# Optimization experiments

Hardware: AMD Instinct MI355X
Metric: run time of the kernel (lower is better)

The kernel has to match this reference:

```python
import jax, jax.numpy as jnp
import numpy as np

KERNEL_SIZE = 5
SIGMA_INTENSITY = 0.1
SIGMA_SPATIAL = 1.0
EPS = 1e-8


def make_spatial_kernel():
    coords = jnp.arange(KERNEL_SIZE, dtype=jnp.float32) - KERNEL_SIZE // 2
    x, y = jnp.meshgrid(coords, coords, indexing='ij')
    return jnp.exp(-(x ** 2 + y ** 2) / (2.0 * SIGMA_SPATIAL ** 2))


def setup_inputs() -> dict:
    key = jax.random.key(0)
    images = jax.random.uniform(key, (16, 3, 512, 512), dtype=jnp.float32)
    spatial_kernel = make_spatial_kernel()
    return {"images": images, "spatial_kernel": spatial_kernel}


def reference(images, spatial_kernel):
    B, C, H, W = images.shape
    K = KERNEL_SIZE
    p = K // 2
    # reflect pad (torch 'reflect' == jnp 'reflect', edge not repeated)
    padded = jnp.pad(images, ((0, 0), (0, 0), (p, p), (p, p)), mode='reflect')
    # extract K*K shifted views -> (B, C, K*K, H, W); fixed small loop over offsets
    patches = jnp.stack(
        [padded[:, :, i:i + H, j:j + W] for i in range(K) for j in range(K)],
        axis=2,
    )
    center_idx = K * K // 2
    center = patches[:, :, center_idx:center_idx + 1, :, :]
    diff = patches - center
    intensity_w = jnp.exp(-(diff ** 2) / (2.0 * SIGMA_INTENSITY ** 2))
    spatial_flat = spatial_kernel.reshape(1, 1, K * K, 1, 1)
    w = spatial_flat * intensity_w
    w = w / (jnp.sum(w, axis=2, keepdims=True) + EPS)
    filtered = jnp.sum(patches * w, axis=2)  # (B, C, H, W)
    return filtered
```

## Files before the change

kernel.cpp:

```cpp
#include <hip/hip_runtime.h>

#define TILE_W 64
#define TILE_H 4
#define HALO   2
#define LW     (TILE_W + 2*HALO)
#define LH     (TILE_H + 2*HALO)
#define IMG    512

__device__ __forceinline__ int reflect_idx(int g) {
    int a = abs(g);
    return min(a, 2 * IMG - 2 - a);
}

#define KS      8.4932184f
#define INV_KS  0.11774083f
#define L2E_HLF 0.72134752f

__global__ __launch_bounds__(256) void bilateral_kernel(
    const float* __restrict__ img, float* __restrict__ out, int planes)
{
    __shared__ float q[LH][LW];

    const int plane = blockIdx.z;
    const int x0 = blockIdx.x * TILE_W;
    const int y0 = blockIdx.y * TILE_H;
    const float* __restrict__ src = img + (size_t)plane * (IMG * IMG);

    const int tid = threadIdx.x + threadIdx.y * TILE_W;

    #pragma unroll
    for (int i = 0; i < 3; ++i) {
        int idx = tid + i * 256;
        if (idx < LH * LW) {
            int r = idx / LW;
            int c = idx - r * LW;
            int gr = reflect_idx(y0 - HALO + r);
            int gc = reflect_idx(x0 - HALO + c);
            q[r][c] = src[gr * IMG + gc] * KS;
        }
    }
    __syncthreads();

    const int tx = threadIdx.x, ty = threadIdx.y;
    const float qc = q[ty + HALO][tx + HALO];

    float wsum = 0.0f, acc = 0.0f;
    #pragma unroll
    for (int dy = 0; dy < 5; ++dy) {
        #pragma unroll
        for (int dx = 0; dx < 5; ++dx) {
            const float ctap = -(float)((dx - 2) * (dx - 2) + (dy - 2) * (dy - 2)) * L2E_HLF;
            float qt  = q[ty + dy][tx + dx];
            float d   = qt - qc;
            float arg = __builtin_fmaf(-d, d, ctap);
            float e   = __builtin_amdgcn_exp2f(arg);
            wsum += e;
            acc = __builtin_fmaf(e, qt, acc);
        }
    }

    float inv = __builtin_amdgcn_rcpf(wsum + 1e-8f);
    out[(size_t)plane * (IMG * IMG) + (size_t)(y0 + ty) * IMG + (x0 + tx)] =
        acc * inv * INV_KS;
}

extern "C" void kernel_launch(void* const* d_in, const int* in_sizes, int n_in,
                              void* d_out, int out_size, void* d_ws, size_t ws_size,
                              hipStream_t stream) {
    const float* img = (const float*)d_in[0];
    float* out = (float*)d_out;
    int planes = in_sizes[0] / (IMG * IMG);
    dim3 grid(IMG / TILE_W, IMG / TILE_H, planes);
    dim3 block(TILE_W, TILE_H, 1);
    bilateral_kernel<<<grid, block, 0, stream>>>(img, out, planes);
}
```

Measured before the change: 150.3 us.

## Compute four rows per thread with register window and packed float2 math

Each thread now produces four vertically adjacent outputs, using a taller tile (16 rows) that loads more halo once per block. Each thread loads an 8x5 window from shared memory into registers and reuses it across its rows. The arithmetic is done on float2 vectors so the compiler can emit packed FP32 ops, and the centre tap is skipped because its weight is known to be 1. The aim is to cut LDS traffic, halo overhead and ALU instructions, at the cost of more registers per thread and fewer blocks.

```diff
diff --git a/kernel.cpp b/kernel.cpp
--- a/kernel.cpp
+++ b/kernel.cpp
@@ -1,11 +1,14 @@
 #include <hip/hip_runtime.h>
 
-#define TILE_W 64
-#define TILE_H 4
-#define HALO   2
-#define LW     (TILE_W + 2*HALO)
-#define LH     (TILE_H + 2*HALO)
-#define IMG    512
+#define IMG  512
+#define TW   64
+#define TH   16
+#define RPT  4
+#define HALO 2
+#define LW   (TW + 2*HALO)
+#define LH   (TH + 2*HALO)
+
+typedef float v2f __attribute__((ext_vector_type(2)));
 
 __device__ __forceinline__ int reflect_idx(int g) {
     int a = abs(g);
@@ -17,51 +20,75 @@
 #define L2E_HLF 0.72134752f
 
 __global__ __launch_bounds__(256) void bilateral_kernel(
-    const float* __restrict__ img, float* __restrict__ out, int planes)
+    const float* __restrict__ img, float* __restrict__ out)
 {
     __shared__ float q[LH][LW];
 
     const int plane = blockIdx.z;
-    const int x0 = blockIdx.x * TILE_W;
-    const int y0 = blockIdx.y * TILE_H;
+    const int x0 = blockIdx.x * TW;
+    const int y0 = blockIdx.y * TH;
     const float* __restrict__ src = img + (size_t)plane * (IMG * IMG);
 
-    const int tid = threadIdx.x + threadIdx.y * TILE_W;
+    const int tid = threadIdx.x + threadIdx.y * 64;
 
     #pragma unroll
-    for (int i = 0; i < 3; ++i) {
+    for (int i = 0; i < 6; ++i) {
         int idx = tid + i * 256;
         if (idx < LH * LW) {
             int r = idx / LW;
             int c = idx - r * LW;
-            int gr = reflect_idx(y0 - HALO + r);
-            int gc = reflect_idx(x0 - HALO + c);
-            q[r][c] = src[gr * IMG + gc] * KS;
+            q[r][c] = src[reflect_idx(y0 - HALO + r) * IMG + reflect_idx(x0 - HALO + c)] * KS;
         }
     }
     __syncthreads();
 
-    const int tx = threadIdx.x, ty = threadIdx.y;
-    const float qc = q[ty + HALO][tx + HALO];
+    const int tx = threadIdx.x;
+    const int ry = threadIdx.y * RPT;
 
-    float wsum = 0.0f, acc = 0.0f;
+    float w[RPT + 4][5];
     #pragma unroll
-    for (int dy = 0; dy < 5; ++dy) {
+    for (int r = 0; r < RPT + 4; ++r)
         #pragma unroll
-        for (int dx = 0; dx < 5; ++dx) {
-            const float ctap = -(float)((dx - 2) * (dx - 2) + (dy - 2) * (dy - 2)) * L2E_HLF;
-            float qt  = q[ty + dy][tx + dx];
-            float d   = qt - qc;
-            float arg = __builtin_fmaf(-d, d, ctap);
-            float e   = __builtin_amdgcn_exp2f(arg);
-            wsum += e;
-            acc = __builtin_fmaf(e, qt, acc);
+        for (int c = 0; c < 5; ++c)
+            w[r][c] = q[ry + r][tx + c];
+
+    float res[RPT];
+    #pragma unroll
+    for (int p = 0; p < RPT; p += 2) {
+        v2f qc;
+        qc.x = w[p + 2][2];
+        qc.y = w[p + 3][2];
+        v2f wsum = {1.0f, 1.0f};
+        v2f acc  = qc;
+
+        #pragma unroll
+        for (int dy = 0; dy < 5; ++dy) {
+            #pragma unroll
+            for (int dx = 0; dx < 5; ++dx) {
+                if (dx == 2 && dy == 2) continue;
+                const float ct = -(float)((dx-2)*(dx-2) + (dy-2)*(dy-2)) * L2E_HLF;
+                const v2f ct2 = {ct, ct};
+                v2f qt;
+                qt.x = w[p + dy][dx];
+                qt.y = w[p + 1 + dy][dx];
+                v2f d   = qt - qc;
+                v2f arg = ct2 - d * d;
+                v2f e;
+                e.x = __builtin_amdgcn_exp2f(arg.x);
+                e.y = __builtin_amdgcn_exp2f(arg.y);
+                wsum += e;
+                acc  += e * qt;
+            }
         }
+        res[p]     = acc.x * __builtin_amdgcn_rcpf(wsum.x + 1e-8f) * INV_KS;
+        res[p + 1] = acc.y * __builtin_amdgcn_rcpf(wsum.y + 1e-8f) * INV_KS;
     }
 
-    float inv = __builtin_amdgcn_rcpf(wsum + 1e-8f);
-    out[(size_t)plane * (IMG * IMG) + (size_t)(y0 + ty) * IMG + (x0 + tx)] =
-        acc * inv * INV_KS;
+    float* dst = out + (size_t)plane * (IMG * IMG)
+                     + (size_t)(y0 + ry) * IMG + (x0 + tx);
+    #pragma unroll
+    for (int r = 0; r < RPT; ++r)
+        dst[r * IMG] = res[r];
 }
 
 extern "C" void kernel_launch(void* const* d_in, const int* in_sizes, int n_in,
@@ -70,7 +97,7 @@
     const float* img = (const float*)d_in[0];
     float* out = (float*)d_out;
     int planes = in_sizes[0] / (IMG * IMG);
-    dim3 grid(IMG / TILE_W, IMG / TILE_H, planes);
-    dim3 block(TILE_W, TILE_H, 1);
-    bilateral_kernel<<<grid, block, 0, stream>>>(img, out, planes);
+    dim3 grid(IMG / TW, IMG / TH, planes);
+    dim3 block(64, 4, 1);
+    bilateral_kernel<<<grid, block, 0, stream>>>(img, out);
 }
```

Result: no change. 149.6 us (-0.5%).

## Register-block bilateral filter with packed FP32 math and bit-trick exponential

Applied to the files above, without the earlier changes.

Replaces the shared-memory tiled kernel with a register-blocked kernel where each thread loads an 8x6 neighbourhood and computes a 2x4 output block using packed FP32 instructions. The exp2 is replaced by a Schraudolph-style integer bit-cast exponential approximation, and the centre tap is folded into the initial sums. Border columns are handled by a separate small edge kernel. This targets the transcendental and ALU cost of the per-tap weight computation, at the cost of approximation error in the weights and a second launch.

```diff
diff --git a/kernel.cpp b/kernel.cpp
--- a/kernel.cpp
+++ b/kernel.cpp
@@ -1,67 +1,111 @@
 #include <hip/hip_runtime.h>
+#include <stdint.h>
 
-#define TILE_W 64
-#define TILE_H 4
-#define HALO   2
-#define LW     (TILE_W + 2*HALO)
-#define LH     (TILE_H + 2*HALO)
-#define IMG    512
+#define IMG 512
+#define KS2 24598.990f
+
+typedef float v2f  __attribute__((ext_vector_type(2)));
+typedef int   v2i  __attribute__((ext_vector_type(2)));
+typedef float v2fu __attribute__((ext_vector_type(2), aligned(4)));
 
 __device__ __forceinline__ int reflect_idx(int g) {
     int a = abs(g);
     return min(a, 2 * IMG - 2 - a);
 }
 
-#define KS      8.4932184f
-#define INV_KS  0.11774083f
-#define L2E_HLF 0.72134752f
+__global__ __launch_bounds__(256, 4) void bilateral_main(
+    const float* __restrict__ img, float* __restrict__ out)
+{
+    const int plane = blockIdx.z;
+    const int pi = blockIdx.x * 64 + threadIdx.x;
+    const int xp = 2 + 2 * pi;
+    if (xp > 508) return;
+    const int yb = (blockIdx.y * 4 + threadIdx.y) * 4;
 
-__global__ __launch_bounds__(256) void bilateral_kernel(
-    const float* __restrict__ img, float* __restrict__ out, int planes)
-{
-    __shared__ float q[LH][LW];
-
-    const int plane = blockIdx.z;
-    const int x0 = blockIdx.x * TILE_W;
-    const int y0 = blockIdx.y * TILE_H;
     const float* __restrict__ src = img + (size_t)plane * (IMG * IMG);
 
-    const int tid = threadIdx.x + threadIdx.y * TILE_W;
+    v2f P[8][5];
+    #pragma unroll
+    for (int r = 0; r < 8; ++r) {
+        const float* rp = src + reflect_idx(yb - 2 + r) * IMG + (xp - 2);
+        #pragma unroll
+        for (int k = 0; k < 5; ++k)
+            P[r][k] = *reinterpret_cast<const v2fu*>(rp + k);
+    }
+
+    const uint32_t ksb = __builtin_bit_cast(uint32_t, KS2);
+    const uint64_t kspair = (uint64_t)ksb * 0x100000001ULL;
+
+    float* const dst = out + (size_t)plane * (IMG * IMG) + (size_t)yb * IMG + xp;
 
     #pragma unroll
-    for (int i = 0; i < 3; ++i) {
-        int idx = tid + i * 256;
-        if (idx < LH * LW) {
-            int r = idx / LW;
-            int c = idx - r * LW;
-            int gr = reflect_idx(y0 - HALO + r);
-            int gc = reflect_idx(x0 - HALO + c);
-            q[r][c] = src[gr * IMG + gc] * KS;
+    for (int p = 0; p < 4; ++p) {
+        v2f qc = P[p + 2][2];
+        v2f qcs;
+        asm("v_pk_mul_f32 %0, %1, %2" : "=v"(qcs) : "s"(kspair), "v"(qc));
+        v2f wsum = {1.0f, 1.0f};
+        v2f acc  = qc;
+
+        #pragma unroll
+        for (int dy = 0; dy < 5; ++dy) {
+            #pragma unroll
+            for (int dx = 0; dx < 5; ++dx) {
+                if (dy == 2 && dx == 2) continue;
+                const int r2 = (dx - 2) * (dx - 2) + (dy - 2) * (dy - 2);
+                const float    Kf    = (float)(1065353216.0 - 6051101.63118 * (double)r2);
+                const uint32_t kb    = __builtin_bit_cast(uint32_t, Kf);
+                const uint64_t kpair = (uint64_t)kb * 0x100000001ULL;
+
+                v2f qt = P[p + dy][dx];
+                v2f ds, t;
+                asm("v_pk_fma_f32 %0, %1, %2, %3 neg_lo:[0,0,1] neg_hi:[0,0,1]"
+                    : "=v"(ds) : "s"(kspair), "v"(qt), "v"(qcs));
+                asm("v_pk_fma_f32 %0, %1, %1, %2 neg_lo:[1,0,0] neg_hi:[1,0,0]"
+                    : "=v"(t) : "v"(ds), "s"(kpair));
+                v2i iv = __builtin_convertvector(t, v2i);
+                v2f e  = __builtin_bit_cast(v2f, iv);
+                asm("v_pk_add_f32 %0, %1, %0" : "+v"(wsum) : "v"(e));
+                asm("v_pk_fma_f32 %0, %1, %2, %0" : "+v"(acc) : "v"(e), "v"(qt));
+            }
         }
+        v2f res;
+        res.x = acc.x * __builtin_amdgcn_rcpf(wsum.x);
+        res.y = acc.y * __builtin_amdgcn_rcpf(wsum.y);
+        *reinterpret_cast<v2f*>(dst + p * IMG) = res;
     }
-    __syncthreads();
+}
 
-    const int tx = threadIdx.x, ty = threadIdx.y;
-    const float qc = q[ty + HALO][tx + HALO];
+__global__ __launch_bounds__(256) void bilateral_edge(
+    const float* __restrict__ img, float* __restrict__ out)
+{
+    const int idx = blockIdx.x * 256 + threadIdx.x;
+    const int plane = idx >> 11;
+    const int rem   = idx & 2047;
+    const int y  = rem >> 2;
+    const int xi = rem & 3;
+    const int x  = (xi < 2) ? xi : (IMG - 4 + xi);
 
-    float wsum = 0.0f, acc = 0.0f;
+    const float* __restrict__ src = img + (size_t)plane * (IMG * IMG);
+    const float qc = src[y * IMG + x];
+    float wsum = 1.0f, acc = qc;
+
     #pragma unroll
     for (int dy = 0; dy < 5; ++dy) {
+        const int yy = reflect_idx(y + dy - 2) * IMG;
         #pragma unroll
         for (int dx = 0; dx < 5; ++dx) {
-            const float ctap = -(float)((dx - 2) * (dx - 2) + (dy - 2) * (dy - 2)) * L2E_HLF;
-            float qt  = q[ty + dy][tx + dx];
-            float d   = qt - qc;
-            float arg = __builtin_fmaf(-d, d, ctap);
-            float e   = __builtin_amdgcn_exp2f(arg);
+            if (dy == 2 && dx == 2) continue;
+            const int r2 = (dx - 2) * (dx - 2) + (dy - 2) * (dy - 2);
+            const float Kf = (float)(1065353216.0 - 6051101.63118 * (double)r2);
+            const float qt = src[yy + reflect_idx(x + dx - 2)];
+            const float d  = (qt - qc) * KS2;
+            const float t  = __builtin_fmaf(-d, d, Kf);
+            const float e  = __builtin_bit_cast(float, (int)t);
             wsum += e;
             acc = __builtin_fmaf(e, qt, acc);
         }
     }
-
-    float inv = __builtin_amdgcn_rcpf(wsum + 1e-8f);
-    out[(size_t)plane * (IMG * IMG) + (size_t)(y0 + ty) * IMG + (x0 + tx)] =
-        acc * inv * INV_KS;
+    out[(size_t)plane * (IMG * IMG) + y * IMG + x] = acc * __builtin_amdgcn_rcpf(wsum);
 }
 
 extern "C" void kernel_launch(void* const* d_in, const int* in_sizes, int n_in,
@@ -69,8 +113,12 @@
                               hipStream_t stream) {
     const float* img = (const float*)d_in[0];
     float* out = (float*)d_out;
-    int planes = in_sizes[0] / (IMG * IMG);
-    dim3 grid(IMG / TILE_W, IMG / TILE_H, planes);
-    dim3 block(TILE_W, TILE_H, 1);
-    bilateral_kernel<<<grid, block, 0, stream>>>(img, out, planes);
+    const int planes = in_sizes[0] / (IMG * IMG);
+
+    dim3 gmain(4, 32, planes);
+    dim3 bmain(64, 4, 1);
+    bilateral_main<<<gmain, bmain, 0, stream>>>(img, out);
+
+    const int edge_threads = planes * IMG * 4;
+    bilateral_edge<<<edge_threads / 256, 256, 0, stream>>>(img, out);
 }
```

Result: faster. 132.3 us (-12.0%).
